# Kernel optimization log

Hardware: AMD Instinct MI355X
Metric: run time of the kernel (lower is better)

Reference implementation:

```python
import jax, jax.numpy as jnp
import numpy as np
import math

L, N, E, H = 2048, 4, 1024, 16  # seq_len, batch, embed_dim, num_heads
HD = E // H                      # head_dim = 64


def setup_inputs() -> dict:
    key = jax.random.key(0)
    ks = jax.random.split(key, 7)
    s = 1.0 / math.sqrt(E)
    return {
        "query": jax.random.normal(ks[0], (L, N, E), jnp.float32),
        "key": jax.random.normal(ks[1], (L, N, E), jnp.float32),
        "value": jax.random.normal(ks[2], (L, N, E), jnp.float32),
        "in_proj_weight": jax.random.normal(ks[3], (3 * E, E), jnp.float32) * s,
        "in_proj_bias": jax.random.normal(ks[4], (3 * E,), jnp.float32) * 0.02,
        "out_proj_weight": jax.random.normal(ks[5], (E, E), jnp.float32) * s,
        "out_proj_bias": jax.random.normal(ks[6], (E,), jnp.float32) * 0.02,
    }


def reference(query, key, value, in_proj_weight, in_proj_bias,
              out_proj_weight, out_proj_bias):
    # --- packed in-projection (q is k is v path of _in_projection_packed) ---
    # F.linear(x, W, b) = x @ W.T + b, W packed as [Wq; Wk; Wv] along dim 0.
    wq, wk, wv = jnp.split(in_proj_weight, 3, axis=0)   # each (E, E)
    bq, bk, bv = jnp.split(in_proj_bias, 3, axis=0)     # each (E,)
    q = query @ wq.T + bq   # (L, N, E)
    k = key @ wk.T + bk
    v = value @ wv.T + bv

    # --- split heads: (L, N, E) -> (N*H, L, HD), matching torch reshape/transpose ---
    def to_heads(x):
        return x.reshape(L, N * H, HD).transpose(1, 0, 2)
    q, k, v = to_heads(q), to_heads(k), to_heads(v)

    # --- scaled dot-product attention (q scaled by 1/sqrt(head_dim)) ---
    q = q / math.sqrt(HD)
    attn = jnp.einsum('bte,bse->bts', q, k)             # (N*H, L, L)
    attn = jax.nn.softmax(attn, axis=-1)
    out = jnp.einsum('bts,bse->bte', attn, v)           # (N*H, L, HD)

    # --- merge heads back to (L, N, E) ---
    out = out.transpose(1, 0, 2).reshape(L, N, E)

    # --- out-projection ---
    out = out @ out_proj_weight.T + out_proj_bias       # (L, N, E)
    return out
```

## Files before the change

### kernel.cpp

```cpp
#include <hip/hip_runtime.h>

using f16 = _Float16;
typedef _Float16 h8 __attribute__((ext_vector_type(8)));
typedef _Float16 h4 __attribute__((ext_vector_type(4)));
typedef float f32x4 __attribute__((ext_vector_type(4)));

constexpr int L_SEQ  = 2048;
constexpr int NBATCH = 4;
constexpr int EMB    = 1024;
constexpr int NHEAD  = 16;
constexpr int HDIM   = 64;
constexpr int BH     = NBATCH * NHEAD;
constexpr int MROWS  = L_SEQ * NBATCH;

#define QSCALE (0.125f * 1.44269504088896341f)

__device__ __forceinline__ void glds16(const void* g, void* l) {
  __builtin_amdgcn_global_load_lds(
      (const __attribute__((address_space(1))) void*)g,
      (__attribute__((address_space(3))) void*)l, 16, 0, 0);
}

__device__ __forceinline__ f32x4 MFMA(h8 a, h8 b, f32x4 c) {
  return __builtin_amdgcn_mfma_f32_16x16x32_f16(a, b, c, 0, 0, 0);
}

__global__ __launch_bounds__(256)
void convert_all_kernel(const float* __restrict__ q, const float* __restrict__ k,
                        const float* __restrict__ v, const float* __restrict__ w,
                        const float* __restrict__ wo,
                        f16* __restrict__ xq, f16* __restrict__ xk, f16* __restrict__ xv,
                        f16* __restrict__ wb, f16* __restrict__ wob) {
  const int NQ  = MROWS * EMB / 4;
  const int NW  = 3 * EMB * EMB / 4;
  const int NWO = EMB * EMB / 4;
  const int total = 3 * NQ + NW + NWO;
  int i = blockIdx.x * blockDim.x + threadIdx.x;
  const int stride = gridDim.x * blockDim.x;
  for (; i < total; i += stride) {
    const float* s; f16* d; int j;
    if      (i <     NQ)      { s = q;  d = xq;  j = i;              }
    else if (i < 2 * NQ)      { s = k;  d = xk;  j = i - NQ;         }
    else if (i < 3 * NQ)      { s = v;  d = xv;  j = i - 2 * NQ;     }
    else if (i < 3 * NQ + NW) { s = w;  d = wb;  j = i - 3 * NQ;     }
    else                      { s = wo; d = wob; j = i - 3 * NQ - NW; }
    float4 t = reinterpret_cast<const float4*>(s)[j];
    h4 o = { (f16)t.x, (f16)t.y, (f16)t.z, (f16)t.w };
    reinterpret_cast<h4*>(d)[j] = o;
  }
}

template<int MODE>
__global__ __launch_bounds__(256)
void gemm_bt(const f16* __restrict__ Abase, const f16* __restrict__ Btbase,
             const float* __restrict__ biasbase, f16* __restrict__ Hbase,
             float* __restrict__ Fout)
{
  const int z = blockIdx.z;
  const f16* A  = Abase  + (size_t)z * MROWS * EMB;
  const f16* Bt = Btbase + (size_t)z * EMB * EMB;
  const float* bias = biasbase + (size_t)z * EMB;

  const int bm = blockIdx.y * 128;
  const int bn = blockIdx.x * 128;
  const int t = threadIdx.x;
  const int w = t >> 6, lane = t & 63;
  const int wr = w >> 1, wc = w & 1;
  const int l16 = lane & 15, g = lane >> 4;

  __shared__ f16 As[128][32];
  __shared__ f16 Bs[128][32];

  f32x4 acc[4][4] = {};

  const int sr  = lane >> 2;
  const int sc8 = (lane & 3) * 8;
  const f16* gA = &A [(size_t)(bm + w*32 + sr) * EMB + sc8];
  const f16* gB = &Bt[(size_t)(bn + w*32 + sr) * EMB + sc8];
  f16* lA0 = &As[w*32][0];
  f16* lA1 = &As[w*32 + 16][0];
  f16* lB0 = &Bs[w*32][0];
  f16* lB1 = &Bs[w*32 + 16][0];

  for (int k0 = 0; k0 < EMB; k0 += 32) {
    __syncthreads();
    glds16(gA + k0, lA0);
    glds16(gA + (size_t)16*EMB + k0, lA1);
    glds16(gB + k0, lB0);
    glds16(gB + (size_t)16*EMB + k0, lB1);
    __syncthreads();

    h8 af[4], bfr[4];
#pragma unroll
    for (int m = 0; m < 4; ++m) af[m]  = *(const h8*)&As[wr*64 + m*16 + l16][g*8];
#pragma unroll
    for (int n = 0; n < 4; ++n) bfr[n] = *(const h8*)&Bs[wc*64 + n*16 + l16][g*8];
    __builtin_amdgcn_s_setprio(1);
#pragma unroll
    for (int m = 0; m < 4; ++m)
#pragma unroll
      for (int n = 0; n < 4; ++n)
        acc[m][n] = __builtin_amdgcn_mfma_f32_16x16x32_f16(af[m], bfr[n], acc[m][n], 0, 0, 0);
    __builtin_amdgcn_s_setprio(0);
  }

#pragma unroll
  for (int m = 0; m < 4; ++m) {
#pragma unroll
    for (int n = 0; n < 4; ++n) {
      const int col = bn + wc*64 + n*16 + l16;
      const float bv = bias[col];
#pragma unroll
      for (int r = 0; r < 4; ++r) {
        const int row = bm + wr*64 + m*16 + g*4 + r;
        float v = acc[m][n][r] + bv;
        if (MODE == 0) {
          if (z == 0) v *= QSCALE;
          const int l = row >> 2, nn = row & 3;
          const int h = col >> 6, hd = col & 63;
          Hbase[(((size_t)z * BH + nn * NHEAD + h) * L_SEQ + l) * HDIM + hd] = (f16)v;
        } else {
          Fout[(size_t)row * EMB + col] = v;
        }
      }
    }
  }
}

__global__ __launch_bounds__(256)
void vtrans_kernel(const f16* __restrict__ V, f16* __restrict__ Vt) {
  const int b = blockIdx.y;
  const int t = threadIdx.x;
  const int d = t & 63;
  const int l0 = (blockIdx.x * 4 + (t >> 6)) * 8;
  const f16* Vb = V  + (size_t)b * L_SEQ * HDIM;
  f16* Vtb      = Vt + (size_t)b * L_SEQ * HDIM;
  h8 v;
#pragma unroll
  for (int i = 0; i < 8; ++i) v[i] = Vb[(size_t)(l0 + i) * HDIM + d];
  *(h8*)&Vtb[(size_t)d * L_SEQ + l0] = v;
}

__device__ __forceinline__ void attn7_step(
    const f16* __restrict__ Kc, const f16* __restrict__ Vc, char* Pw,
    const h8 (&qf)[2][2],
    f32x4 (&o)[2][4], f32x4 (&osum)[2],
    int l16, int g)
{
  const int sw = (l16 & 7) << 3;

  h8 kf[4][2];
#pragma unroll
  for (int kt = 0; kt < 4; ++kt)
#pragma unroll
    for (int kk = 0; kk < 2; ++kk)
      kf[kt][kk] = *(const h8*)&Kc[(kt*16 + l16)*64 + ((kk*32 + g*8) ^ sw)];

  f32x4 st[2][4];
  __builtin_amdgcn_s_setprio(1);
#pragma unroll
  for (int kt = 0; kt < 4; ++kt)
#pragma unroll
    for (int qt = 0; qt < 2; ++qt) {
      f32x4 zz = {};
      zz = MFMA(kf[kt][0], qf[qt][0], zz);
      st[qt][kt] = MFMA(kf[kt][1], qf[qt][1], zz);
    }
  __builtin_amdgcn_s_setprio(0);

  h8 vf[4][2];
#pragma unroll
  for (int dt = 0; dt < 4; ++dt)
#pragma unroll
    for (int c = 0; c < 2; ++c)
      vf[dt][c] = *(const h8*)&Vc[(dt*16 + l16)*64 + ((c*32 + g*8) ^ sw)];

  const h8 ones = { (f16)1, (f16)1, (f16)1, (f16)1, (f16)1, (f16)1, (f16)1, (f16)1 };

#pragma unroll
  for (int qt = 0; qt < 2; ++qt) {
#pragma unroll
    for (int kt = 0; kt < 4; ++kt) {
      h4 pv = { (f16)__builtin_amdgcn_exp2f(st[qt][kt][0]),
                (f16)__builtin_amdgcn_exp2f(st[qt][kt][1]),
                (f16)__builtin_amdgcn_exp2f(st[qt][kt][2]),
                (f16)__builtin_amdgcn_exp2f(st[qt][kt][3]) };
      const int byteoff = (l16*128 + (kt*16 + g*4)*2) ^ ((l16 & 7) << 4);
      *(h4*)(Pw + byteoff) = pv;
    }
#pragma unroll
    for (int c = 0; c < 2; ++c) {
      const int byteoff = (l16*128 + c*64 + g*16) ^ ((l16 & 7) << 4);
      h8 pf = *(const h8*)(Pw + byteoff);
      __builtin_amdgcn_s_setprio(1);
      osum[qt] = MFMA(pf, ones, osum[qt]);
#pragma unroll
      for (int dt = 0; dt < 4; ++dt)
        o[qt][dt] = MFMA(pf, vf[dt][c], o[qt][dt]);
      __builtin_amdgcn_s_setprio(0);
    }
  }
}

__global__ __launch_bounds__(256, 3)
void attn7_kernel(const f16* __restrict__ Qh, const f16* __restrict__ Kh,
                  const f16* __restrict__ Vt, f16* __restrict__ AO)
{
  const int id = blockIdx.x;
  const int b    = (id & 7) | ((id >> 7) << 3);
  const int qblk = (id >> 3) & 15;

  const int t = threadIdx.x;
  const int w = t >> 6, lane = t & 63;
  const int l16 = lane & 15, g = lane >> 4;

  const f16* Qb = Qh + (size_t)b * L_SEQ * HDIM;
  const f16* Kb = Kh + (size_t)b * L_SEQ * HDIM;
  const f16* Vb = Vt + (size_t)b * (size_t)HDIM * L_SEQ;

  __shared__ f16 Ks[2][64*64];
  __shared__ f16 Vs[2][64*64];
  __shared__ f16 Plds[4][1024];
  char* Pw = (char*)&Plds[w][0];

  const int q0 = qblk * 128 + w * 32;

  h8 qf[2][2];
#pragma unroll
  for (int qt = 0; qt < 2; ++qt)
#pragma unroll
    for (int kk = 0; kk < 2; ++kk)
      qf[qt][kk] = *(const h8*)&Qb[(size_t)(q0 + qt*16 + l16) * HDIM + kk*32 + g*8];

  const int srow = lane >> 3;
  const int scol = 8 * ((lane & 7) ^ srow);
  const int r0   = w*16 + srow;
  const f16* gK0 = Kb + (size_t)(r0    ) * HDIM + scol;
  const f16* gK1 = Kb + (size_t)(r0 + 8) * HDIM + scol;
  const f16* gV0 = Vb + (size_t)(r0    ) * L_SEQ + scol;
  const f16* gV1 = Vb + (size_t)(r0 + 8) * L_SEQ + scol;
  const int ldsw = w * 1024;

  f32x4 o[2][4] = {};
  f32x4 osum[2] = {};

  glds16(gK0, &Ks[0][ldsw]);
  glds16(gK1, &Ks[0][ldsw + 512]);
  glds16(gV0, &Vs[0][ldsw]);
  glds16(gV1, &Vs[0][ldsw + 512]);
  __syncthreads();

#pragma unroll 1
  for (int j0 = 0; j0 < L_SEQ; j0 += 128) {
    {
      const int jn = (j0 + 64) & (L_SEQ - 1);
      glds16(gK0 + (size_t)jn * HDIM, &Ks[1][ldsw]);
      glds16(gK1 + (size_t)jn * HDIM, &Ks[1][ldsw + 512]);
      glds16(gV0 + jn, &Vs[1][ldsw]);
      glds16(gV1 + jn, &Vs[1][ldsw + 512]);
      attn7_step(&Ks[0][0], &Vs[0][0], Pw, qf, o, osum, l16, g);
      __syncthreads();
    }
    {
      const int jn = (j0 + 128) & (L_SEQ - 1);
      glds16(gK0 + (size_t)jn * HDIM, &Ks[0][ldsw]);
      glds16(gK1 + (size_t)jn * HDIM, &Ks[0][ldsw + 512]);
      glds16(gV0 + jn, &Vs[0][ldsw]);
      glds16(gV1 + jn, &Vs[0][ldsw + 512]);
      attn7_step(&Ks[1][0], &Vs[1][0], Pw, qf, o, osum, l16, g);
      __syncthreads();
    }
  }

  const int nn = b >> 4, h = b & 15;
#pragma unroll
  for (int qt = 0; qt < 2; ++qt) {
#pragma unroll
    for (int r = 0; r < 4; ++r) {
      const float iv = 1.0f / osum[qt][r];
      const int lr = q0 + qt*16 + g*4 + r;
#pragma unroll
      for (int dt = 0; dt < 4; ++dt)
        AO[((size_t)lr * NBATCH + nn) * EMB + h*HDIM + dt*16 + l16] = (f16)(o[qt][dt][r] * iv);
    }
  }
}

extern "C" void kernel_launch(void* const* d_in, const int* in_sizes, int n_in,
                              void* d_out, int out_size, void* d_ws, size_t ws_size,
                              hipStream_t stream) {
  const float* query = (const float*)d_in[0];
  const float* key   = (const float*)d_in[1];
  const float* value = (const float*)d_in[2];
  const float* in_w  = (const float*)d_in[3];
  const float* in_b  = (const float*)d_in[4];
  const float* out_w = (const float*)d_in[5];
  const float* out_b = (const float*)d_in[6];
  float* out = (float*)d_out;

  char* ws = (char*)d_ws;
  size_t offH  = 0;
  size_t offX  = offH  + (size_t)3 * BH * L_SEQ * HDIM * 2;
  size_t offW  = offX  + (size_t)3 * MROWS * EMB * 2;
  size_t offWo = offW  + (size_t)3 * EMB * EMB * 2;
  size_t offAO = offWo + (size_t)EMB * EMB * 2;
  f16* Hbase = (f16*)(ws + offH);
  f16* Xb    = (f16*)(ws + offX);
  f16* Wb    = (f16*)(ws + offW);
  f16* Wob   = (f16*)(ws + offWo);
  f16* AOb   = (f16*)(ws + offAO);
  f16* Vtb   = Xb;

  hipLaunchKernelGGL(convert_all_kernel, dim3(2048), dim3(256), 0, stream,
                     query, key, value, in_w, out_w,
                     Xb + 0 * (size_t)MROWS * EMB,
                     Xb + 1 * (size_t)MROWS * EMB,
                     Xb + 2 * (size_t)MROWS * EMB,
                     Wb, Wob);

  hipLaunchKernelGGL((gemm_bt<0>), dim3(EMB/128, MROWS/128, 3), dim3(256), 0, stream,
                     Xb, Wb, in_b, Hbase, (float*)nullptr);

  f16* Vh = Hbase + (size_t)2 * BH * L_SEQ * HDIM;
  hipLaunchKernelGGL(vtrans_kernel, dim3(L_SEQ/32, BH), dim3(256), 0, stream, Vh, Vtb);

  hipLaunchKernelGGL(attn7_kernel, dim3(L_SEQ/128 * BH), dim3(256), 0, stream,
                     Hbase,
                     Hbase + (size_t)BH * L_SEQ * HDIM,
                     Vtb, AOb);

  hipLaunchKernelGGL((gemm_bt<1>), dim3(EMB/128, MROWS/128, 1), dim3(256), 0, stream,
                     AOb, Wob, out_b, (f16*)nullptr, out);
}
```

Baseline: 229.2 us.

## Rewrite attention inner loop with 32x32 MFMA and register-resident P via permlane swap

The attention step now uses 32x32x16 MFMA tiles instead of 16x16x32, computing S transposed so each lane holds 16 score values. Exponentiated scores are packed to half precision and rearranged in registers with v_permlane32_swap, so they can feed the PV MFMA directly. This removes the LDS round-trip for P and the extra ones-vector MFMA used for row sums. Row sums are accumulated in scalar registers and combined with shuffles at the end. The catch is higher register pressure and reliance on the exact MFMA output layout for correctness.

```diff
diff --git a/kernel.cpp b/kernel.cpp
--- a/kernel.cpp
+++ b/kernel.cpp
@@ -4,6 +4,8 @@
 typedef _Float16 h8 __attribute__((ext_vector_type(8)));
 typedef _Float16 h4 __attribute__((ext_vector_type(4)));
 typedef float f32x4 __attribute__((ext_vector_type(4)));
+typedef float f32x16 __attribute__((ext_vector_type(16)));
+typedef unsigned u32x4 __attribute__((ext_vector_type(4)));
 
 constexpr int L_SEQ  = 2048;
 constexpr int NBATCH = 4;
@@ -23,6 +25,13 @@
 
 __device__ __forceinline__ f32x4 MFMA(h8 a, h8 b, f32x4 c) {
   return __builtin_amdgcn_mfma_f32_16x16x32_f16(a, b, c, 0, 0, 0);
+}
+__device__ __forceinline__ f32x16 MFMA32(h8 a, h8 b, f32x16 c) {
+  return __builtin_amdgcn_mfma_f32_32x32x16_f16(a, b, c, 0, 0, 0);
+}
+__device__ __forceinline__ unsigned pkrtz(float x, float y) {
+  auto t = __builtin_amdgcn_cvt_pkrtz(x, y);
+  return __builtin_bit_cast(unsigned, t);
 }
 
 __global__ __launch_bounds__(256)
@@ -141,69 +150,64 @@
   *(h8*)&Vtb[(size_t)d * L_SEQ + l0] = v;
 }
 
-__device__ __forceinline__ void attn7_step(
-    const f16* __restrict__ Kc, const f16* __restrict__ Vc, char* Pw,
-    const h8 (&qf)[2][2],
-    f32x4 (&o)[2][4], f32x4 (&osum)[2],
-    int l16, int g)
+__device__ __forceinline__ void attn8_step(
+    const f16* __restrict__ Kc, const f16* __restrict__ Vc,
+    const h8 (&qf)[4],
+    f32x16 (&o)[2], float (&psum)[4],
+    int l31, int hi)
 {
-  const int sw = (l16 & 7) << 3;
-
-  h8 kf[4][2];
-#pragma unroll
-  for (int kt = 0; kt < 4; ++kt)
-#pragma unroll
-    for (int kk = 0; kk < 2; ++kk)
-      kf[kt][kk] = *(const h8*)&Kc[(kt*16 + l16)*64 + ((kk*32 + g*8) ^ sw)];
-
-  f32x4 st[2][4];
+  const int swz = (l31 & 7) << 3;
+
+  h8 vf[4][2];
+#pragma unroll
+  for (int s2 = 0; s2 < 4; ++s2)
+#pragma unroll
+    for (int dt = 0; dt < 2; ++dt)
+      vf[s2][dt] = *(const h8*)&Vc[(dt*32 + l31)*64 + ((s2*16 + hi*8) ^ swz)];
+
+  h8 pa[4];
+#pragma unroll
+  for (int kt = 0; kt < 2; ++kt) {
+    f32x16 acc = {};
+    __builtin_amdgcn_s_setprio(1);
+#pragma unroll
+    for (int s = 0; s < 4; ++s) {
+      h8 kf = *(const h8*)&Kc[(kt*32 + l31)*64 + ((s*16 + hi*8) ^ swz)];
+      acc = MFMA32(kf, qf[s], acc);
+    }
+    __builtin_amdgcn_s_setprio(0);
+
+    float p[16];
+#pragma unroll
+    for (int r = 0; r < 16; ++r) p[r] = __builtin_amdgcn_exp2f(acc[r]);
+#pragma unroll
+    for (int r = 0; r < 16; ++r) psum[r & 3] += p[r];
+
+#pragma unroll
+    for (int half = 0; half < 2; ++half) {
+      const int b0 = half * 8;
+      unsigned A = pkrtz(p[b0+0], p[b0+1]);
+      unsigned C = pkrtz(p[b0+2], p[b0+3]);
+      unsigned B = pkrtz(p[b0+4], p[b0+5]);
+      unsigned D = pkrtz(p[b0+6], p[b0+7]);
+      asm("v_permlane32_swap_b32 %0, %1" : "+v"(A), "+v"(B));
+      asm("v_permlane32_swap_b32 %0, %1" : "+v"(C), "+v"(D));
+      u32x4 wv = { A, C, B, D };
+      pa[kt*2 + half] = __builtin_bit_cast(h8, wv);
+    }
+  }
+
   __builtin_amdgcn_s_setprio(1);
 #pragma unroll
-  for (int kt = 0; kt < 4; ++kt)
-#pragma unroll
-    for (int qt = 0; qt < 2; ++qt) {
-      f32x4 zz = {};
-      zz = MFMA(kf[kt][0], qf[qt][0], zz);
-      st[qt][kt] = MFMA(kf[kt][1], qf[qt][1], zz);
-    }
+  for (int s2 = 0; s2 < 4; ++s2) {
+    o[0] = MFMA32(pa[s2], vf[s2][0], o[0]);
+    o[1] = MFMA32(pa[s2], vf[s2][1], o[1]);
+  }
   __builtin_amdgcn_s_setprio(0);
-
-  h8 vf[4][2];
-#pragma unroll
-  for (int dt = 0; dt < 4; ++dt)
-#pragma unroll
-    for (int c = 0; c < 2; ++c)
-      vf[dt][c] = *(const h8*)&Vc[(dt*16 + l16)*64 + ((c*32 + g*8) ^ sw)];
-
-  const h8 ones = { (f16)1, (f16)1, (f16)1, (f16)1, (f16)1, (f16)1, (f16)1, (f16)1 };
-
-#pragma unroll
-  for (int qt = 0; qt < 2; ++qt) {
-#pragma unroll
-    for (int kt = 0; kt < 4; ++kt) {
-      h4 pv = { (f16)__builtin_amdgcn_exp2f(st[qt][kt][0]),
-                (f16)__builtin_amdgcn_exp2f(st[qt][kt][1]),
-                (f16)__builtin_amdgcn_exp2f(st[qt][kt][2]),
-                (f16)__builtin_amdgcn_exp2f(st[qt][kt][3]) };
-      const int byteoff = (l16*128 + (kt*16 + g*4)*2) ^ ((l16 & 7) << 4);
-      *(h4*)(Pw + byteoff) = pv;
-    }
-#pragma unroll
-    for (int c = 0; c < 2; ++c) {
-      const int byteoff = (l16*128 + c*64 + g*16) ^ ((l16 & 7) << 4);
-      h8 pf = *(const h8*)(Pw + byteoff);
-      __builtin_amdgcn_s_setprio(1);
-      osum[qt] = MFMA(pf, ones, osum[qt]);
-#pragma unroll
-      for (int dt = 0; dt < 4; ++dt)
-        o[qt][dt] = MFMA(pf, vf[dt][c], o[qt][dt]);
-      __builtin_amdgcn_s_setprio(0);
-    }
-  }
 }
 
 __global__ __launch_bounds__(256, 3)
-void attn7_kernel(const f16* __restrict__ Qh, const f16* __restrict__ Kh,
+void attn8_kernel(const f16* __restrict__ Qh, const f16* __restrict__ Kh,
                   const f16* __restrict__ Vt, f16* __restrict__ AO)
 {
   const int id = blockIdx.x;
@@ -212,7 +216,7 @@
 
   const int t = threadIdx.x;
   const int w = t >> 6, lane = t & 63;
-  const int l16 = lane & 15, g = lane >> 4;
+  const int l31 = lane & 31, hi = lane >> 5;
 
   const f16* Qb = Qh + (size_t)b * L_SEQ * HDIM;
   const f16* Kb = Kh + (size_t)b * L_SEQ * HDIM;
@@ -220,17 +224,13 @@
 
   __shared__ f16 Ks[2][64*64];
   __shared__ f16 Vs[2][64*64];
-  __shared__ f16 Plds[4][1024];
-  char* Pw = (char*)&Plds[w][0];
 
   const int q0 = qblk * 128 + w * 32;
 
-  h8 qf[2][2];
-#pragma unroll
-  for (int qt = 0; qt < 2; ++qt)
-#pragma unroll
-    for (int kk = 0; kk < 2; ++kk)
-      qf[qt][kk] = *(const h8*)&Qb[(size_t)(q0 + qt*16 + l16) * HDIM + kk*32 + g*8];
+  h8 qf[4];
+#pragma unroll
+  for (int s = 0; s < 4; ++s)
+    qf[s] = *(const h8*)&Qb[(size_t)(q0 + l31) * HDIM + s*16 + hi*8];
 
   const int srow = lane >> 3;
   const int scol = 8 * ((lane & 7) ^ srow);
@@ -241,8 +241,8 @@
   const f16* gV1 = Vb + (size_t)(r0 + 8) * L_SEQ + scol;
   const int ldsw = w * 1024;
 
-  f32x4 o[2][4] = {};
-  f32x4 osum[2] = {};
+  f32x16 o[2] = {};
+  float psum[4] = { 0.f, 0.f, 0.f, 0.f };
 
   glds16(gK0, &Ks[0][ldsw]);
   glds16(gK1, &Ks[0][ldsw + 512]);
@@ -258,7 +258,7 @@
       glds16(gK1 + (size_t)jn * HDIM, &Ks[1][ldsw + 512]);
       glds16(gV0 + jn, &Vs[1][ldsw]);
       glds16(gV1 + jn, &Vs[1][ldsw + 512]);
-      attn7_step(&Ks[0][0], &Vs[0][0], Pw, qf, o, osum, l16, g);
+      attn8_step(&Ks[0][0], &Vs[0][0], qf, o, psum, l31, hi);
       __syncthreads();
     }
     {
@@ -267,22 +267,25 @@
       glds16(gK1 + (size_t)jn * HDIM, &Ks[0][ldsw + 512]);
       glds16(gV0 + jn, &Vs[0][ldsw]);
       glds16(gV1 + jn, &Vs[0][ldsw + 512]);
-      attn7_step(&Ks[1][0], &Vs[1][0], Pw, qf, o, osum, l16, g);
+      attn8_step(&Ks[1][0], &Vs[1][0], qf, o, psum, l31, hi);
       __syncthreads();
     }
   }
 
+  float ssum = (psum[0] + psum[1]) + (psum[2] + psum[3]);
+  ssum += __shfl_xor(ssum, 32);
+  const float inv = 1.0f / ssum;
+
   const int nn = b >> 4, h = b & 15;
 #pragma unroll
-  for (int qt = 0; qt < 2; ++qt) {
-#pragma unroll
-    for (int r = 0; r < 4; ++r) {
-      const float iv = 1.0f / osum[qt][r];
-      const int lr = q0 + qt*16 + g*4 + r;
-#pragma unroll
-      for (int dt = 0; dt < 4; ++dt)
-        AO[((size_t)lr * NBATCH + nn) * EMB + h*HDIM + dt*16 + l16] = (f16)(o[qt][dt][r] * iv);
-    }
+  for (int r = 0; r < 16; ++r) {
+    const int qrow = (r & 3) + 8 * (r >> 2) + 4 * hi;
+    const float iv = __shfl(inv, qrow);
+    const int lr = q0 + qrow;
+#pragma unroll
+    for (int dt = 0; dt < 2; ++dt)
+      AO[((size_t)lr * NBATCH + nn) * EMB + h*HDIM + dt*32 + l31] =
+          (f16)(o[dt][r] * iv);
   }
 }
 
@@ -324,7 +327,7 @@
   f16* Vh = Hbase + (size_t)2 * BH * L_SEQ * HDIM;
   hipLaunchKernelGGL(vtrans_kernel, dim3(L_SEQ/32, BH), dim3(256), 0, stream, Vh, Vtb);
 
-  hipLaunchKernelGGL(attn7_kernel, dim3(L_SEQ/128 * BH), dim3(256), 0, stream,
+  hipLaunchKernelGGL(attn8_kernel, dim3(L_SEQ/128 * BH), dim3(256), 0, stream,
                      Hbase,
                      Hbase + (size_t)BH * L_SEQ * HDIM,
                      Vtb, AOb);
```

New measurement: 232.9 us. Within noise of the previous version (+1.6%).
